# Kernel tuning notes

Measured on AMD Instinct MI355X. Metric: run time of the kernel, lower is better.

The kernel has to match this reference:

```python
import math
import jax, jax.numpy as jnp
import numpy as np

N, E = 20000, 640000
S_DIM, Z_DIM, H, QK, VD = 64, 64, 4, 8, 8
EPS = 1e-8


def quat_rotate(v, q):
    # v: [..., 3], q: [..., 4] (w, x, y, z), broadcastable. Unit-quaternion rotation:
    # v' = v + 2*(w*(u x v) + u x (u x v))
    w = q[..., 0:1]
    u = q[..., 1:4]
    uv = jnp.cross(u, v)
    return v + 2.0 * (w * uv + jnp.cross(u, uv))


def setup_inputs() -> dict:
    key = jax.random.key(0)
    ks = jax.random.split(key, 16)
    s = jax.random.normal(ks[0], (N, S_DIM), dtype=jnp.float32)
    z = jax.random.normal(ks[1], (E, Z_DIM), dtype=jnp.float32)
    edge_index = jax.random.randint(ks[2], (2, E), 0, N)
    quaternion = jax.random.normal(ks[3], (N, 4), dtype=jnp.float32)
    quaternion = quaternion / jnp.linalg.norm(quaternion, axis=-1, keepdims=True)
    translation = jax.random.normal(ks[4], (N, 3), dtype=jnp.float32)
    sc_s = 1.0 / math.sqrt(S_DIM)
    sc_z = 1.0 / math.sqrt(Z_DIM)
    # weights stored [in, out] so y = x @ W (equivalent to torch x @ W.T)
    Wq_s = jax.random.normal(ks[5], (S_DIM, H * S_DIM), dtype=jnp.float32) * sc_s
    Wk_s = jax.random.normal(ks[6], (S_DIM, H * S_DIM), dtype=jnp.float32) * sc_s
    Wv_s = jax.random.normal(ks[7], (S_DIM, H * S_DIM), dtype=jnp.float32) * sc_s
    Wq_v = jax.random.normal(ks[8], (S_DIM, H * QK * 3), dtype=jnp.float32) * sc_s
    Wk_v = jax.random.normal(ks[9], (S_DIM, H * QK * 3), dtype=jnp.float32) * sc_s
    Wv_v = jax.random.normal(ks[10], (S_DIM, H * VD * 3), dtype=jnp.float32) * sc_s
    Wb = jax.random.normal(ks[11], (Z_DIM, H), dtype=jnp.float32) * sc_z
    bb = jnp.zeros((H,), dtype=jnp.float32)
    Wdz = jax.random.normal(ks[12], (Z_DIM, Z_DIM // 4), dtype=jnp.float32) * sc_z
    bdz = jnp.zeros((Z_DIM // 4,), dtype=jnp.float32)
    head_weights = jnp.full((H,), 0.541324854612918, dtype=jnp.float32)  # softplus^{-1}(1)
    concat_dim = Z_DIM // 4 + S_DIM + VD * 4
    Wout = jax.random.normal(ks[13], (H * concat_dim, S_DIM), dtype=jnp.float32) / math.sqrt(H * concat_dim)
    bout = jnp.zeros((S_DIM,), dtype=jnp.float32)
    return {
        's': s, 'z': z, 'edge_index': edge_index, 'quaternion': quaternion,
        'translation': translation, 'Wq_s': Wq_s, 'Wk_s': Wk_s, 'Wv_s': Wv_s,
        'Wq_v': Wq_v, 'Wk_v': Wk_v, 'Wv_v': Wv_v, 'Wb': Wb, 'bb': bb,
        'Wdz': Wdz, 'bdz': bdz, 'head_weights': head_weights,
        'Wout': Wout, 'bout': bout,
    }


def reference(s, z, edge_index, quaternion, translation,
              Wq_s, Wk_s, Wv_s, Wq_v, Wk_v, Wv_v,
              Wb, bb, Wdz, bdz, head_weights, Wout, bout):
    idx_i, idx_j = edge_index[0], edge_index[1]
    n = s.shape[0]
    h = head_weights.shape[0]
    qk = Wq_v.shape[1] // (3 * h)
    vd = Wv_v.shape[1] // (3 * h)

    q_scalar = (s @ Wq_s).reshape(n, h, -1)
    k_scalar = (s @ Wk_s).reshape(n, h, -1)
    v_scalar = (s @ Wv_s).reshape(n, h, -1)

    def to_points(x):
        # torch.split into 3 chunks then stack(dim=-1): [n, 3*c] -> [n, c, 3]
        c = x.shape[-1] // 3
        return jnp.swapaxes(x.reshape(n, 3, c), 1, 2)

    quat_b = quaternion[:, None, :]
    trans_b = translation[:, None, :]
    q_vec = (quat_rotate(to_points(s @ Wq_v), quat_b) + trans_b).reshape(n, h, qk, 3)
    k_vec = (quat_rotate(to_points(s @ Wk_v), quat_b) + trans_b).reshape(n, h, qk, 3)
    v_vec = (quat_rotate(to_points(s @ Wv_v), quat_b) + trans_b).reshape(n, h, vd, 3)

    b_bias = z @ Wb + bb  # [E, H]

    attn = jnp.sum(k_scalar[idx_i] * q_scalar[idx_j], axis=-1)  # [E, H]
    attn = attn * math.sqrt(1.0 / 3 * qk) + math.sqrt(1.0 / 3) * b_bias

    disp = q_vec[idx_i] - k_vec[idx_j]            # [E, H, qk, 3]
    vec_att = jnp.sum(disp * disp, axis=-1)       # [E, H, qk]
    hw = jax.nn.softplus(head_weights)[None, :, None]
    vec_att = jnp.sum(vec_att * hw, axis=-1) * math.sqrt(1.0 / (3 * (qk * 9.0 / 2))) * (-0.5)
    attn = attn + vec_att

    # segment softmax over destination node idx_i
    seg_max = jax.ops.segment_max(attn, idx_i, num_segments=n)
    ea = jnp.exp(attn - seg_max[idx_i])
    denom = jax.ops.segment_sum(ea, idx_i, num_segments=n)
    attn = ea / denom[idx_i]                      # [E, H]

    out_scalar = jax.ops.segment_sum(attn[:, :, None] * v_scalar[idx_i], idx_i, num_segments=n)
    out_scalar = out_scalar.reshape(n, -1)

    out_vec = jax.ops.segment_sum(attn[:, :, None, None] * v_vec[idx_i], idx_i, num_segments=n)
    out_vec = out_vec - translation[:, None, None, :]
    q_conj = jnp.concatenate([quaternion[:, :1], -quaternion[:, 1:]], axis=-1)
    out_vec = quat_rotate(out_vec, q_conj[:, None, None, :])   # [n, h, vd, 3]
    out_vec_norm = jnp.sqrt(jnp.sum(out_vec * out_vec, axis=-1) + EPS).reshape(n, -1)
    out_vec_flat = out_vec.reshape(n, -1, 3)

    pair_z = z @ Wdz + bdz                         # [E, z/4]
    out_pair = jax.ops.segment_sum(attn[:, :, None] * pair_z[:, None, :], idx_i, num_segments=n)
    out_pair = out_pair.reshape(n, -1)

    feats = jnp.concatenate([out_scalar,
                             out_vec_flat[..., 0], out_vec_flat[..., 1], out_vec_flat[..., 2],
                             out_vec_norm, out_pair], axis=-1)
    return feats @ Wout + bout
```

## Files before the change

### kernel.cpp

```cpp
#include <hip/hip_runtime.h>
#include <stdint.h>


#define C_SQRT83  1.6329931618554518f
#define C_SQRT13  0.5773502691896258f
#define C_VEC    -0.04811252243246881f

__device__ __forceinline__ unsigned short f2bf(float f){
  unsigned u = __float_as_uint(f);
  u += 0x7fffu + ((u >> 16) & 1u);
  return (unsigned short)(u >> 16);
}
__device__ __forceinline__ unsigned pack2(float a, float b){
  return (unsigned)f2bf(a) | ((unsigned)f2bf(b) << 16);
}
__device__ __forceinline__ float bflo(unsigned u){ return __uint_as_float(u << 16); }
__device__ __forceinline__ float bfhi(unsigned u){ return __uint_as_float(u & 0xffff0000u); }

__device__ __forceinline__ void quat_rot(float w, float ux, float uy, float uz,
                                         float vx, float vy, float vz,
                                         float& ox, float& oy, float& oz){
  float cx = uy*vz - uz*vy;
  float cy = uz*vx - ux*vz;
  float cz = ux*vy - uy*vx;
  float dx = uy*cz - uz*cy;
  float dy = uz*cx - ux*cz;
  float dz = ux*cy - uy*cx;
  ox = vx + 2.f*(w*cx + dx);
  oy = vy + 2.f*(w*cy + dy);
  oz = vz + 2.f*(w*cz + dz);
}


__global__ __launch_bounds__(256) void k_zero(unsigned* __restrict__ counts, int n){
  int g = blockIdx.x*256 + threadIdx.x;
  if (g < n) counts[g] = 0u;
}

__global__ __launch_bounds__(256) void k_count(const int* __restrict__ ei,
                                               unsigned* __restrict__ counts, int ne){
  int e = blockIdx.x*256 + threadIdx.x;
  if (e >= ne) return;
  atomicAdd(&counts[ei[e]], 1u);
}

__global__ __launch_bounds__(256) void k_scan(const unsigned* __restrict__ counts,
                                              unsigned* __restrict__ row_off,
                                              unsigned* __restrict__ cursor, int n){
  __shared__ unsigned part[256];
  int t = threadIdx.x;
  int chunk = (n + 255) >> 8;
  int s0 = t*chunk, s1 = min(s0 + chunk, n);
  unsigned sum = 0;
  for (int k = s0; k < s1; ++k) sum += counts[k];
  part[t] = sum; __syncthreads();
  for (int off = 1; off < 256; off <<= 1){
    unsigned v = (t >= off) ? part[t-off] : 0u;
    __syncthreads();
    part[t] += v;
    __syncthreads();
  }
  unsigned run = (t == 0) ? 0u : part[t-1];
  for (int k = s0; k < s1; ++k){
    row_off[k] = run; cursor[k] = run; run += counts[k];
  }
  if (t == 255) row_off[n] = part[255];
}

__global__ __launch_bounds__(256) void k_fill(const int* __restrict__ ei,
                                              unsigned* __restrict__ cursor,
                                              unsigned* __restrict__ si,
                                              unsigned* __restrict__ sj,
                                              unsigned* __restrict__ se, int ne){
  int e = blockIdx.x*256 + threadIdx.x;
  if (e >= ne) return;
  int i = ei[e];
  unsigned pos = atomicAdd(&cursor[i], 1u);
  si[pos] = (unsigned)i;
  sj[pos] = (unsigned)ei[ne + e];
  se[pos] = (unsigned)e;
}


#define BN 32

__device__ __forceinline__ void pass256(const float* __restrict__ W,
                                        const float st[BN][66], int cg, int sl,
                                        float acc[8][4]){
  #pragma unroll
  for (int i=0;i<8;i++){ acc[i][0]=0.f; acc[i][1]=0.f; acc[i][2]=0.f; acc[i][3]=0.f; }
  #pragma unroll 4
  for (int k = 0; k < 64; ++k){
    const float4 w = *(const float4*)(W + (size_t)k*256 + cg*4);
    #pragma unroll
    for (int i=0;i<8;i++){
      const float sv = st[sl*8+i][k];
      acc[i][0] += sv*w.x; acc[i][1] += sv*w.y; acc[i][2] += sv*w.z; acc[i][3] += sv*w.w;
    }
  }
}

__device__ __forceinline__ void pass96(const float* __restrict__ W,
                                       const float st[BN][66], int cgp, int slp,
                                       float acc[4][4]){
  #pragma unroll
  for (int i=0;i<4;i++){ acc[i][0]=0.f; acc[i][1]=0.f; acc[i][2]=0.f; acc[i][3]=0.f; }
  if (cgp >= 24) return;
  #pragma unroll 4
  for (int k = 0; k < 64; ++k){
    const float4 w = *(const float4*)(W + (size_t)k*96 + cgp*4);
    #pragma unroll
    for (int i=0;i<4;i++){
      const float sv = st[slp*4+i][k];
      acc[i][0] += sv*w.x; acc[i][1] += sv*w.y; acc[i][2] += sv*w.z; acc[i][3] += sv*w.w;
    }
  }
}

__global__ __launch_bounds__(256) void k_proj(
    const float* __restrict__ s, const float* __restrict__ quat, const float* __restrict__ trans,
    const float* __restrict__ Wqs, const float* __restrict__ Wks, const float* __restrict__ Wvs,
    const float* __restrict__ Wqv, const float* __restrict__ Wkv, const float* __restrict__ Wvv,
    unsigned* __restrict__ qs, unsigned* __restrict__ ks, float* __restrict__ vs,
    unsigned* __restrict__ qv, unsigned* __restrict__ kv, float* __restrict__ vv, int n)
{
  __shared__ float st[BN][66];
  __shared__ float pt[BN][97];
  const int tid = threadIdx.x;
  const int node0 = blockIdx.x * BN;

  #pragma unroll
  for (int r = 0; r < 2; ++r){
    const int idx = tid + r*256;
    const int nd = idx >> 4, c4 = idx & 15;
    const int g = node0 + nd;
    float4 v = make_float4(0.f,0.f,0.f,0.f);
    if (g < n) v = *(const float4*)(s + (size_t)g*64 + c4*4);
    st[nd][c4*4+0]=v.x; st[nd][c4*4+1]=v.y; st[nd][c4*4+2]=v.z; st[nd][c4*4+3]=v.w;
  }
  __syncthreads();

  const int cg = tid & 63, sl = tid >> 6;
  const int cgp = tid & 31, slp = tid >> 5;
  float acc[8][4];

  pass256(Wqs, st, cg, sl, acc);
  #pragma unroll
  for (int i=0;i<8;i++){
    const int g = node0 + sl*8 + i;
    if (g < n){
      uint2 u; u.x = pack2(acc[i][0],acc[i][1]); u.y = pack2(acc[i][2],acc[i][3]);
      *(uint2*)(qs + (size_t)g*128 + cg*2) = u;
    }
  }
  pass256(Wks, st, cg, sl, acc);
  #pragma unroll
  for (int i=0;i<8;i++){
    const int g = node0 + sl*8 + i;
    if (g < n){
      uint2 u; u.x = pack2(acc[i][0],acc[i][1]); u.y = pack2(acc[i][2],acc[i][3]);
      *(uint2*)(ks + (size_t)g*128 + cg*2) = u;
    }
  }
  pass256(Wvs, st, cg, sl, acc);
  #pragma unroll
  for (int i=0;i<8;i++){
    const int g = node0 + sl*8 + i;
    if (g < n){
      float4 f; f.x=acc[i][0]; f.y=acc[i][1]; f.z=acc[i][2]; f.w=acc[i][3];
      *(float4*)(vs + (size_t)g*256 + cg*4) = f;
    }
  }

  float pac[4][4];

  pass96(Wqv, st, cgp, slp, pac);
  __syncthreads();
  if (cgp < 24){
    #pragma unroll
    for (int i=0;i<4;i++){
      #pragma unroll
      for (int c=0;c<4;c++) pt[slp*4+i][cgp*4+c] = pac[i][c];
    }
  }
  __syncthreads();
  #pragma unroll
  for (int r = 0; r < 2; ++r){
    const int t2 = tid + r*256;
    const int nd = t2 >> 4, pp = t2 & 15;
    const int g = node0 + nd;
    if (g < n){
      const float4 q4 = *(const float4*)(quat + (size_t)g*4);
      const float tx = trans[(size_t)g*3], ty = trans[(size_t)g*3+1], tz = trans[(size_t)g*3+2];
      float x0,y0,z0,x1,y1,z1;
      quat_rot(q4.x,q4.y,q4.z,q4.w, pt[nd][2*pp],   pt[nd][32+2*pp],   pt[nd][64+2*pp],   x0,y0,z0);
      quat_rot(q4.x,q4.y,q4.z,q4.w, pt[nd][2*pp+1], pt[nd][32+2*pp+1], pt[nd][64+2*pp+1], x1,y1,z1);
      x0+=tx; y0+=ty; z0+=tz; x1+=tx; y1+=ty; z1+=tz;
      unsigned* d = qv + (size_t)g*48 + pp*3;
      d[0] = pack2(x0,y0); d[1] = pack2(z0,x1); d[2] = pack2(y1,z1);
    }
  }

  pass96(Wkv, st, cgp, slp, pac);
  __syncthreads();
  if (cgp < 24){
    #pragma unroll
    for (int i=0;i<4;i++){
      #pragma unroll
      for (int c=0;c<4;c++) pt[slp*4+i][cgp*4+c] = pac[i][c];
    }
  }
  __syncthreads();
  #pragma unroll
  for (int r = 0; r < 2; ++r){
    const int t2 = tid + r*256;
    const int nd = t2 >> 4, pp = t2 & 15;
    const int g = node0 + nd;
    if (g < n){
      const float4 q4 = *(const float4*)(quat + (size_t)g*4);
      const float tx = trans[(size_t)g*3], ty = trans[(size_t)g*3+1], tz = trans[(size_t)g*3+2];
      float x0,y0,z0,x1,y1,z1;
      quat_rot(q4.x,q4.y,q4.z,q4.w, pt[nd][2*pp],   pt[nd][32+2*pp],   pt[nd][64+2*pp],   x0,y0,z0);
      quat_rot(q4.x,q4.y,q4.z,q4.w, pt[nd][2*pp+1], pt[nd][32+2*pp+1], pt[nd][64+2*pp+1], x1,y1,z1);
      x0+=tx; y0+=ty; z0+=tz; x1+=tx; y1+=ty; z1+=tz;
      unsigned* d = kv + (size_t)g*48 + pp*3;
      d[0] = pack2(x0,y0); d[1] = pack2(z0,x1); d[2] = pack2(y1,z1);
    }
  }

  pass96(Wvv, st, cgp, slp, pac);
  __syncthreads();
  if (cgp < 24){
    #pragma unroll
    for (int i=0;i<4;i++){
      #pragma unroll
      for (int c=0;c<4;c++) pt[slp*4+i][cgp*4+c] = pac[i][c];
    }
  }
  __syncthreads();
  #pragma unroll
  for (int r = 0; r < 12; ++r){
    const int idx = tid + r*256;
    const int nd = idx / 96, col = idx - nd*96;
    const int g = node0 + nd;
    if (g < n) vv[(size_t)g*96 + col] = pt[nd][col];
  }
}


__global__ __launch_bounds__(256) void k_edge(
    const float* __restrict__ z,
    const unsigned* __restrict__ si, const unsigned* __restrict__ sj, const unsigned* __restrict__ se,
    const float* __restrict__ Wb,  const float* __restrict__ bb,
    const float* __restrict__ Wdz, const float* __restrict__ bdz,
    const float* __restrict__ hwts,
    const unsigned* __restrict__ qs, const unsigned* __restrict__ ks,
    const unsigned* __restrict__ qv, const unsigned* __restrict__ kv,
    float* __restrict__ logits, unsigned* __restrict__ pz, int ne)
{
  const int p = blockIdx.x*256 + threadIdx.x;
  if (p >= ne) return;
  const unsigned i = si[p], j = sj[p], e = se[p];

  float b4[4];  b4[0]=b4[1]=b4[2]=b4[3]=0.f;
  float pacc[16];
  #pragma unroll
  for (int c=0;c<16;c++) pacc[c]=0.f;
  const float* zr = z + (size_t)e*64;
  #pragma unroll
  for (int k4 = 0; k4 < 16; ++k4){
    const float4 zv = *(const float4*)(zr + 4*k4);
    #pragma unroll
    for (int kk = 0; kk < 4; ++kk){
      const int k = 4*k4 + kk;
      const float zk = (kk==0)?zv.x:((kk==1)?zv.y:((kk==2)?zv.z:zv.w));
      const float4 wb = *(const float4*)(Wb + k*4);
      b4[0]+=zk*wb.x; b4[1]+=zk*wb.y; b4[2]+=zk*wb.z; b4[3]+=zk*wb.w;
      const float* wd = Wdz + k*16;
      const float4 w0=*(const float4*)(wd), w1=*(const float4*)(wd+4),
                   w2=*(const float4*)(wd+8), w3=*(const float4*)(wd+12);
      pacc[ 0]+=zk*w0.x; pacc[ 1]+=zk*w0.y; pacc[ 2]+=zk*w0.z; pacc[ 3]+=zk*w0.w;
      pacc[ 4]+=zk*w1.x; pacc[ 5]+=zk*w1.y; pacc[ 6]+=zk*w1.z; pacc[ 7]+=zk*w1.w;
      pacc[ 8]+=zk*w2.x; pacc[ 9]+=zk*w2.y; pacc[10]+=zk*w2.z; pacc[11]+=zk*w2.w;
      pacc[12]+=zk*w3.x; pacc[13]+=zk*w3.y; pacc[14]+=zk*w3.z; pacc[15]+=zk*w3.w;
    }
  }
  #pragma unroll
  for (int c=0;c<16;c++) pacc[c] += bdz[c];
  { uint4 u0, u1;
    u0.x=pack2(pacc[0],pacc[1]);   u0.y=pack2(pacc[2],pacc[3]);
    u0.z=pack2(pacc[4],pacc[5]);   u0.w=pack2(pacc[6],pacc[7]);
    u1.x=pack2(pacc[8],pacc[9]);   u1.y=pack2(pacc[10],pacc[11]);
    u1.z=pack2(pacc[12],pacc[13]); u1.w=pack2(pacc[14],pacc[15]);
    uint4* d = (uint4*)(pz + (size_t)p*8);
    d[0]=u0; d[1]=u1; }

  const uint4* kr = (const uint4*)(ks + (size_t)i*128);
  const uint4* qr = (const uint4*)(qs + (size_t)j*128);
  float sdot[4];
  #pragma unroll
  for (int h = 0; h < 4; ++h){
    float acc = 0.f;
    #pragma unroll
    for (int c = 0; c < 8; ++c){
      const uint4 a = kr[h*8+c];
      const uint4 b = qr[h*8+c];
      acc += bflo(a.x)*bflo(b.x) + bfhi(a.x)*bfhi(b.x);
      acc += bflo(a.y)*bflo(b.y) + bfhi(a.y)*bfhi(b.y);
      acc += bflo(a.z)*bflo(b.z) + bfhi(a.z)*bfhi(b.z);
      acc += bflo(a.w)*bflo(b.w) + bfhi(a.w)*bfhi(b.w);
    }
    sdot[h] = acc;
  }

  const uint4* qvr = (const uint4*)(qv + (size_t)i*48);
  const uint4* kvr = (const uint4*)(kv + (size_t)j*48);
  float vsum[4];
  #pragma unroll
  for (int h = 0; h < 4; ++h){
    float acc = 0.f;
    #pragma unroll
    for (int c = 0; c < 3; ++c){
      const uint4 a = qvr[h*3+c];
      const uint4 b = kvr[h*3+c];
      float d;
      d = bflo(a.x)-bflo(b.x); acc += d*d;  d = bfhi(a.x)-bfhi(b.x); acc += d*d;
      d = bflo(a.y)-bflo(b.y); acc += d*d;  d = bfhi(a.y)-bfhi(b.y); acc += d*d;
      d = bflo(a.z)-bflo(b.z); acc += d*d;  d = bfhi(a.z)-bfhi(b.z); acc += d*d;
      d = bflo(a.w)-bflo(b.w); acc += d*d;  d = bfhi(a.w)-bfhi(b.w); acc += d*d;
    }
    vsum[h] = acc;
  }

  float4 lg;
  {
    float l[4];
    #pragma unroll
    for (int h = 0; h < 4; ++h){
      const float hw = log1pf(__expf(hwts[h]));
      l[h] = C_SQRT83*sdot[h] + C_SQRT13*(b4[h] + bb[h]) + C_VEC*hw*vsum[h];
    }
    lg.x=l[0]; lg.y=l[1]; lg.z=l[2]; lg.w=l[3];
  }
  *(float4*)(logits + (size_t)p*4) = lg;
}


__global__ __launch_bounds__(256) void k_soft(
    const float* __restrict__ logits, const unsigned* __restrict__ pz,
    const unsigned* __restrict__ row_off, float* __restrict__ out_pair, int n)
{
  const int t = blockIdx.x*256 + threadIdx.x;
  if (t >= n*4) return;
  const int i = t >> 2, h = t & 3;
  const int beg = (int)row_off[i], end = (int)row_off[i+1];

  float m = -3.4e38f;
  for (int p = beg; p < end; ++p) m = fmaxf(m, logits[(size_t)p*4 + h]);

  float ssum = 0.f;
  float acc[16];
  #pragma unroll
  for (int c=0;c<16;c++) acc[c]=0.f;

  for (int p = beg; p < end; ++p){
    const float w = __expf(logits[(size_t)p*4 + h] - m);
    ssum += w;
    const uint4* pr = (const uint4*)(pz + (size_t)p*8);
    const uint4 a = pr[0], b = pr[1];
    acc[ 0]+=w*bflo(a.x); acc[ 1]+=w*bfhi(a.x);
    acc[ 2]+=w*bflo(a.y); acc[ 3]+=w*bfhi(a.y);
    acc[ 4]+=w*bflo(a.z); acc[ 5]+=w*bfhi(a.z);
    acc[ 6]+=w*bflo(a.w); acc[ 7]+=w*bfhi(a.w);
    acc[ 8]+=w*bflo(b.x); acc[ 9]+=w*bfhi(b.x);
    acc[10]+=w*bflo(b.y); acc[11]+=w*bfhi(b.y);
    acc[12]+=w*bflo(b.z); acc[13]+=w*bfhi(b.z);
    acc[14]+=w*bflo(b.w); acc[15]+=w*bfhi(b.w);
  }
  const float inv = (end > beg) ? (1.f/ssum) : 0.f;
  float4* dst = (float4*)(out_pair + (size_t)i*64 + h*16);
  float4 o;
  o.x=acc[0]*inv;  o.y=acc[1]*inv;  o.z=acc[2]*inv;  o.w=acc[3]*inv;  dst[0]=o;
  o.x=acc[4]*inv;  o.y=acc[5]*inv;  o.z=acc[6]*inv;  o.w=acc[7]*inv;  dst[1]=o;
  o.x=acc[8]*inv;  o.y=acc[9]*inv;  o.z=acc[10]*inv; o.w=acc[11]*inv; dst[2]=o;
  o.x=acc[12]*inv; o.y=acc[13]*inv; o.z=acc[14]*inv; o.w=acc[15]*inv; dst[3]=o;
}


__global__ __launch_bounds__(256) void k_out(
    const float* __restrict__ vs, const float* __restrict__ vv,
    const float* __restrict__ out_pair, const unsigned* __restrict__ row_off,
    const float* __restrict__ quat, const float* __restrict__ trans,
    const float* __restrict__ Wout, const float* __restrict__ bout,
    float* __restrict__ out, int n)
{
  __shared__ float feats[32][448];
  __shared__ int degs[32];
  const int tid = threadIdx.x;
  const int node0 = blockIdx.x*32;

  if (tid < 32){
    const int g = node0 + tid;
    degs[tid] = (g < n) ? (int)(row_off[g+1] - row_off[g]) : 1;
  }
  __syncthreads();

  for (int x = tid; x < 32*256; x += 256){
    const int nd = x >> 8, c = x & 255;
    const int g = node0 + nd;
    feats[nd][c] = (g < n && degs[nd] > 0) ? vs[(size_t)g*256 + c] : 0.f;
  }
  for (int x = tid; x < 32*64; x += 256){
    const int nd = x >> 6, c = x & 63;
    const int g = node0 + nd;
    feats[nd][384 + c] = (g < n) ? out_pair[(size_t)g*64 + c] : 0.f;
  }
  for (int x = tid; x < 32*32; x += 256){
    const int nd = x >> 5, pt = x & 31;
    const int g = node0 + nd;
    float X=0.f, Y=0.f, Z=0.f;
    if (g < n){
      if (degs[nd] > 0){
        X = vv[(size_t)g*96 + pt];
        Y = vv[(size_t)g*96 + 32 + pt];
        Z = vv[(size_t)g*96 + 64 + pt];
      } else {
        const float4 q4 = *(const float4*)(quat + (size_t)g*4);
        const float tx = trans[(size_t)g*3], ty = trans[(size_t)g*3+1], tz = trans[(size_t)g*3+2];
        quat_rot(q4.x, -q4.y, -q4.z, -q4.w, -tx, -ty, -tz, X, Y, Z);
      }
    }
    feats[nd][256 + pt] = X;
    feats[nd][288 + pt] = Y;
    feats[nd][320 + pt] = Z;
    feats[nd][352 + pt] = sqrtf(X*X + Y*Y + Z*Z + 1e-8f);
  }
  __syncthreads();

  const int lane = tid & 63;
  const int wave = tid >> 6;
  float acc[8];
  #pragma unroll
  for (int q8=0;q8<8;q8++) acc[q8]=0.f;

  for (int k = 0; k < 448; ++k){
    const float wv = Wout[(size_t)k*64 + lane];
    #pragma unroll
    for (int q8 = 0; q8 < 8; ++q8)
      acc[q8] += feats[wave*8 + q8][k] * wv;
  }
  const float bo = bout[lane];
  #pragma unroll
  for (int q8 = 0; q8 < 8; ++q8){
    const int g = node0 + wave*8 + q8;
    if (g < n) out[(size_t)g*64 + lane] = acc[q8] + bo;
  }
}


extern "C" void kernel_launch(void* const* d_in, const int* in_sizes, int n_in,
                              void* d_out, int out_size, void* d_ws, size_t ws_size,
                              hipStream_t stream) {
  const float* s     = (const float*)d_in[0];
  const float* z     = (const float*)d_in[1];
  const int*   ei    = (const int*)  d_in[2];
  const float* quat  = (const float*)d_in[3];
  const float* trans = (const float*)d_in[4];
  const float* Wqs   = (const float*)d_in[5];
  const float* Wks   = (const float*)d_in[6];
  const float* Wvs   = (const float*)d_in[7];
  const float* Wqv   = (const float*)d_in[8];
  const float* Wkv   = (const float*)d_in[9];
  const float* Wvv   = (const float*)d_in[10];
  const float* Wb    = (const float*)d_in[11];
  const float* bb    = (const float*)d_in[12];
  const float* Wdz   = (const float*)d_in[13];
  const float* bdz   = (const float*)d_in[14];
  const float* hwts  = (const float*)d_in[15];
  const float* Wout  = (const float*)d_in[16];
  const float* bout  = (const float*)d_in[17];
  float* out = (float*)d_out;

  const int n  = in_sizes[0] / 64;
  const int ne = in_sizes[1] / 64;

  size_t off = 0;
  char* base = (char*)d_ws;
  auto take = [&](size_t bytes)->char* {
    char* p = base + off;
    off += (bytes + 255) & ~(size_t)255;
    return p;
  };
  unsigned* qs     = (unsigned*)take((size_t)n*512);
  unsigned* ks     = (unsigned*)take((size_t)n*512);
  unsigned* qvt    = (unsigned*)take((size_t)n*192);
  unsigned* kvt    = (unsigned*)take((size_t)n*192);
  float*    vs     = (float*)   take((size_t)n*1024);
  float*    vv     = (float*)   take((size_t)n*384);
  float*    logits = (float*)   take((size_t)ne*16);
  unsigned* pz     = (unsigned*)take((size_t)ne*32);
  unsigned* counts = (unsigned*)take((size_t)n*4);
  unsigned* roff   = (unsigned*)take((size_t)(n+1)*4);
  unsigned* cur    = (unsigned*)take((size_t)n*4);
  unsigned* si     = (unsigned*)take((size_t)ne*4);
  unsigned* sj     = (unsigned*)take((size_t)ne*4);
  unsigned* se     = (unsigned*)take((size_t)ne*4);
  float*    opair  = (float*)   take((size_t)n*256);
  (void)ws_size; (void)n_in; (void)out_size;

  const int gbE = (ne + 255) / 256;
  const int gbN = (n  + 255) / 256;

  k_zero <<<gbN, 256, 0, stream>>>(counts, n);
  k_count<<<gbE, 256, 0, stream>>>(ei, counts, ne);
  k_scan <<<1,   256, 0, stream>>>(counts, roff, cur, n);
  k_fill <<<gbE, 256, 0, stream>>>(ei, cur, si, sj, se, ne);
  k_proj <<<(n + BN - 1)/BN, 256, 0, stream>>>(s, quat, trans, Wqs, Wks, Wvs, Wqv, Wkv, Wvv,
                                               qs, ks, vs, qvt, kvt, vv, n);
  k_edge <<<gbE, 256, 0, stream>>>(z, si, sj, se, Wb, bb, Wdz, bdz, hwts,
                                   qs, ks, qvt, kvt, logits, pz, ne);
  k_soft <<<(n*4 + 255)/256, 256, 0, stream>>>(logits, pz, roff, opair, n);
  k_out  <<<(n + 31)/32, 256, 0, stream>>>(vs, vv, opair, roff, quat, trans,
                                           Wout, bout, out, n);
}
```

Baseline: 688.1 us.

## Use wave-per-node softmax, atomic-free CSR fill, transposed smem projection, vectorized output GEMV

The CSR build now records each edge's rank from the counting atomic, so the fill step computes positions without a second atomic pass. The zero kernel is replaced by hipMemsetAsync. The projection kernel stores node features transposed in shared memory so it can use float4 LDS reads. The segment softmax now gives each node a full wave with shuffle reductions instead of one thread per (node, head), which spreads work more evenly but computes exp more than once per edge. The output GEMV reads four feature values at a time as float4.

```diff
diff --git a/kernel.cpp b/kernel.cpp
--- a/kernel.cpp
+++ b/kernel.cpp
@@ -32,21 +32,16 @@
 }
 
 
-__global__ __launch_bounds__(256) void k_zero(unsigned* __restrict__ counts, int n){
-  int g = blockIdx.x*256 + threadIdx.x;
-  if (g < n) counts[g] = 0u;
-}
-
 __global__ __launch_bounds__(256) void k_count(const int* __restrict__ ei,
-                                               unsigned* __restrict__ counts, int ne){
+                                               unsigned* __restrict__ counts,
+                                               unsigned* __restrict__ rank, int ne){
   int e = blockIdx.x*256 + threadIdx.x;
   if (e >= ne) return;
-  atomicAdd(&counts[ei[e]], 1u);
+  rank[e] = atomicAdd(&counts[ei[e]], 1u);
 }
 
 __global__ __launch_bounds__(256) void k_scan(const unsigned* __restrict__ counts,
-                                              unsigned* __restrict__ row_off,
-                                              unsigned* __restrict__ cursor, int n){
+                                              unsigned* __restrict__ row_off, int n){
   __shared__ unsigned part[256];
   int t = threadIdx.x;
   int chunk = (n + 255) >> 8;
@@ -62,20 +57,21 @@
   }
   unsigned run = (t == 0) ? 0u : part[t-1];
   for (int k = s0; k < s1; ++k){
-    row_off[k] = run; cursor[k] = run; run += counts[k];
+    row_off[k] = run; run += counts[k];
   }
   if (t == 255) row_off[n] = part[255];
 }
 
 __global__ __launch_bounds__(256) void k_fill(const int* __restrict__ ei,
-                                              unsigned* __restrict__ cursor,
+                                              const unsigned* __restrict__ rank,
+                                              const unsigned* __restrict__ roff,
                                               unsigned* __restrict__ si,
                                               unsigned* __restrict__ sj,
                                               unsigned* __restrict__ se, int ne){
   int e = blockIdx.x*256 + threadIdx.x;
   if (e >= ne) return;
-  int i = ei[e];
-  unsigned pos = atomicAdd(&cursor[i], 1u);
+  const int i = ei[e];
+  const unsigned pos = roff[i] + rank[e];
   si[pos] = (unsigned)i;
   sj[pos] = (unsigned)ei[ne + e];
   se[pos] = (unsigned)e;
@@ -85,23 +81,28 @@
 #define BN 32
 
 __device__ __forceinline__ void pass256(const float* __restrict__ W,
-                                        const float st[BN][66], int cg, int sl,
+                                        const float stT[64][40], int cg, int sl,
                                         float acc[8][4]){
   #pragma unroll
   for (int i=0;i<8;i++){ acc[i][0]=0.f; acc[i][1]=0.f; acc[i][2]=0.f; acc[i][3]=0.f; }
   #pragma unroll 4
   for (int k = 0; k < 64; ++k){
-    const float4 w = *(const float4*)(W + (size_t)k*256 + cg*4);
-    #pragma unroll
-    for (int i=0;i<8;i++){
-      const float sv = st[sl*8+i][k];
-      acc[i][0] += sv*w.x; acc[i][1] += sv*w.y; acc[i][2] += sv*w.z; acc[i][3] += sv*w.w;
-    }
+    const float4 w  = *(const float4*)(W + (size_t)k*256 + cg*4);
+    const float4 n0 = *(const float4*)&stT[k][sl*8];
+    const float4 n1 = *(const float4*)&stT[k][sl*8+4];
+    acc[0][0]+=n0.x*w.x; acc[0][1]+=n0.x*w.y; acc[0][2]+=n0.x*w.z; acc[0][3]+=n0.x*w.w;
+    acc[1][0]+=n0.y*w.x; acc[1][1]+=n0.y*w.y; acc[1][2]+=n0.y*w.z; acc[1][3]+=n0.y*w.w;
+    acc[2][0]+=n0.z*w.x; acc[2][1]+=n0.z*w.y; acc[2][2]+=n0.z*w.z; acc[2][3]+=n0.z*w.w;
+    acc[3][0]+=n0.w*w.x; acc[3][1]+=n0.w*w.y; acc[3][2]+=n0.w*w.z; acc[3][3]+=n0.w*w.w;
+    acc[4][0]+=n1.x*w.x; acc[4][1]+=n1.x*w.y; acc[4][2]+=n1.x*w.z; acc[4][3]+=n1.x*w.w;
+    acc[5][0]+=n1.y*w.x; acc[5][1]+=n1.y*w.y; acc[5][2]+=n1.y*w.z; acc[5][3]+=n1.y*w.w;
+    acc[6][0]+=n1.z*w.x; acc[6][1]+=n1.z*w.y; acc[6][2]+=n1.z*w.z; acc[6][3]+=n1.z*w.w;
+    acc[7][0]+=n1.w*w.x; acc[7][1]+=n1.w*w.y; acc[7][2]+=n1.w*w.z; acc[7][3]+=n1.w*w.w;
   }
 }
 
 __device__ __forceinline__ void pass96(const float* __restrict__ W,
-                                       const float st[BN][66], int cgp, int slp,
+                                       const float stT[64][40], int cgp, int slp,
                                        float acc[4][4]){
   #pragma unroll
   for (int i=0;i<4;i++){ acc[i][0]=0.f; acc[i][1]=0.f; acc[i][2]=0.f; acc[i][3]=0.f; }
@@ -109,11 +110,11 @@
   #pragma unroll 4
   for (int k = 0; k < 64; ++k){
     const float4 w = *(const float4*)(W + (size_t)k*96 + cgp*4);
-    #pragma unroll
-    for (int i=0;i<4;i++){
-      const float sv = st[slp*4+i][k];
-      acc[i][0] += sv*w.x; acc[i][1] += sv*w.y; acc[i][2] += sv*w.z; acc[i][3] += sv*w.w;
-    }
+    const float4 nv = *(const float4*)&stT[k][slp*4];
+    acc[0][0]+=nv.x*w.x; acc[0][1]+=nv.x*w.y; acc[0][2]+=nv.x*w.z; acc[0][3]+=nv.x*w.w;
+    acc[1][0]+=nv.y*w.x; acc[1][1]+=nv.y*w.y; acc[1][2]+=nv.y*w.z; acc[1][3]+=nv.y*w.w;
+    acc[2][0]+=nv.z*w.x; acc[2][1]+=nv.z*w.y; acc[2][2]+=nv.z*w.z; acc[2][3]+=nv.z*w.w;
+    acc[3][0]+=nv.w*w.x; acc[3][1]+=nv.w*w.y; acc[3][2]+=nv.w*w.z; acc[3][3]+=nv.w*w.w;
   }
 }
 
@@ -124,7 +125,7 @@
     unsigned* __restrict__ qs, unsigned* __restrict__ ks, float* __restrict__ vs,
     unsigned* __restrict__ qv, unsigned* __restrict__ kv, float* __restrict__ vv, int n)
 {
-  __shared__ float st[BN][66];
+  __shared__ float stT[64][40];
   __shared__ float pt[BN][97];
   const int tid = threadIdx.x;
   const int node0 = blockIdx.x * BN;
@@ -136,7 +137,7 @@
     const int g = node0 + nd;
     float4 v = make_float4(0.f,0.f,0.f,0.f);
     if (g < n) v = *(const float4*)(s + (size_t)g*64 + c4*4);
-    st[nd][c4*4+0]=v.x; st[nd][c4*4+1]=v.y; st[nd][c4*4+2]=v.z; st[nd][c4*4+3]=v.w;
+    stT[c4*4+0][nd]=v.x; stT[c4*4+1][nd]=v.y; stT[c4*4+2][nd]=v.z; stT[c4*4+3][nd]=v.w;
   }
   __syncthreads();
 
@@ -144,7 +145,7 @@
   const int cgp = tid & 31, slp = tid >> 5;
   float acc[8][4];
 
-  pass256(Wqs, st, cg, sl, acc);
+  pass256(Wqs, stT, cg, sl, acc);
   #pragma unroll
   for (int i=0;i<8;i++){
     const int g = node0 + sl*8 + i;
@@ -153,7 +154,7 @@
       *(uint2*)(qs + (size_t)g*128 + cg*2) = u;
     }
   }
-  pass256(Wks, st, cg, sl, acc);
+  pass256(Wks, stT, cg, sl, acc);
   #pragma unroll
   for (int i=0;i<8;i++){
     const int g = node0 + sl*8 + i;
@@ -162,7 +163,7 @@
       *(uint2*)(ks + (size_t)g*128 + cg*2) = u;
     }
   }
-  pass256(Wvs, st, cg, sl, acc);
+  pass256(Wvs, stT, cg, sl, acc);
   #pragma unroll
   for (int i=0;i<8;i++){
     const int g = node0 + sl*8 + i;
@@ -174,7 +175,7 @@
 
   float pac[4][4];
 
-  pass96(Wqv, st, cgp, slp, pac);
+  pass96(Wqv, stT, cgp, slp, pac);
   __syncthreads();
   if (cgp < 24){
     #pragma unroll
@@ -201,7 +202,7 @@
     }
   }
 
-  pass96(Wkv, st, cgp, slp, pac);
+  pass96(Wkv, stT, cgp, slp, pac);
   __syncthreads();
   if (cgp < 24){
     #pragma unroll
@@ -228,7 +229,7 @@
     }
   }
 
-  pass96(Wvv, st, cgp, slp, pac);
+  pass96(Wvv, stT, cgp, slp, pac);
   __syncthreads();
   if (cgp < 24){
     #pragma unroll
@@ -350,40 +351,57 @@
     const float* __restrict__ logits, const unsigned* __restrict__ pz,
     const unsigned* __restrict__ row_off, float* __restrict__ out_pair, int n)
 {
-  const int t = blockIdx.x*256 + threadIdx.x;
-  if (t >= n*4) return;
-  const int i = t >> 2, h = t & 3;
-  const int beg = (int)row_off[i], end = (int)row_off[i+1];
-
-  float m = -3.4e38f;
-  for (int p = beg; p < end; ++p) m = fmaxf(m, logits[(size_t)p*4 + h]);
-
-  float ssum = 0.f;
-  float acc[16];
-  #pragma unroll
-  for (int c=0;c<16;c++) acc[c]=0.f;
-
-  for (int p = beg; p < end; ++p){
-    const float w = __expf(logits[(size_t)p*4 + h] - m);
-    ssum += w;
-    const uint4* pr = (const uint4*)(pz + (size_t)p*8);
-    const uint4 a = pr[0], b = pr[1];
-    acc[ 0]+=w*bflo(a.x); acc[ 1]+=w*bfhi(a.x);
-    acc[ 2]+=w*bflo(a.y); acc[ 3]+=w*bfhi(a.y);
-    acc[ 4]+=w*bflo(a.z); acc[ 5]+=w*bfhi(a.z);
-    acc[ 6]+=w*bflo(a.w); acc[ 7]+=w*bfhi(a.w);
-    acc[ 8]+=w*bflo(b.x); acc[ 9]+=w*bfhi(b.x);
-    acc[10]+=w*bflo(b.y); acc[11]+=w*bfhi(b.y);
-    acc[12]+=w*bflo(b.z); acc[13]+=w*bfhi(b.z);
-    acc[14]+=w*bflo(b.w); acc[15]+=w*bfhi(b.w);
-  }
-  const float inv = (end > beg) ? (1.f/ssum) : 0.f;
-  float4* dst = (float4*)(out_pair + (size_t)i*64 + h*16);
-  float4 o;
-  o.x=acc[0]*inv;  o.y=acc[1]*inv;  o.z=acc[2]*inv;  o.w=acc[3]*inv;  dst[0]=o;
-  o.x=acc[4]*inv;  o.y=acc[5]*inv;  o.z=acc[6]*inv;  o.w=acc[7]*inv;  dst[1]=o;
-  o.x=acc[8]*inv;  o.y=acc[9]*inv;  o.z=acc[10]*inv; o.w=acc[11]*inv; dst[2]=o;
-  o.x=acc[12]*inv; o.y=acc[13]*inv; o.z=acc[14]*inv; o.w=acc[15]*inv; dst[3]=o;
+  const int node = blockIdx.x*4 + (threadIdx.x >> 6);
+  if (node >= n) return;
+  const int lane = threadIdx.x & 63;
+  const int beg = (int)row_off[node], end = (int)row_off[node+1];
+
+  float m[4] = {-3.0e38f,-3.0e38f,-3.0e38f,-3.0e38f};
+  for (int p = beg + lane; p < end; p += 64){
+    const float4 l = *(const float4*)(logits + (size_t)p*4);
+    m[0]=fmaxf(m[0],l.x); m[1]=fmaxf(m[1],l.y); m[2]=fmaxf(m[2],l.z); m[3]=fmaxf(m[3],l.w);
+  }
+  #pragma unroll
+  for (int msk = 1; msk < 64; msk <<= 1){
+    #pragma unroll
+    for (int h=0;h<4;h++) m[h] = fmaxf(m[h], __shfl_xor(m[h], msk));
+  }
+  float S[4] = {0.f,0.f,0.f,0.f};
+  for (int p = beg + lane; p < end; p += 64){
+    const float4 l = *(const float4*)(logits + (size_t)p*4);
+    S[0]+=__expf(l.x-m[0]); S[1]+=__expf(l.y-m[1]);
+    S[2]+=__expf(l.z-m[2]); S[3]+=__expf(l.w-m[3]);
+  }
+  #pragma unroll
+  for (int msk = 1; msk < 64; msk <<= 1){
+    #pragma unroll
+    for (int h=0;h<4;h++) S[h] += __shfl_xor(S[h], msk);
+  }
+  float inv[4];
+  #pragma unroll
+  for (int h=0;h<4;h++) inv[h] = (S[h] > 0.f) ? (1.f/S[h]) : 0.f;
+
+  const int e4 = lane >> 4, c = lane & 15;
+  float acc[4] = {0.f,0.f,0.f,0.f};
+  for (int base = beg; base < end; base += 4){
+    const int p = base + e4;
+    if (p < end){
+      const float4 l = *(const float4*)(logits + (size_t)p*4);
+      const unsigned u = pz[(size_t)p*8 + (c>>1)];
+      const float pzv = (c & 1) ? bfhi(u) : bflo(u);
+      acc[0] += __expf(l.x-m[0]) * pzv;
+      acc[1] += __expf(l.y-m[1]) * pzv;
+      acc[2] += __expf(l.z-m[2]) * pzv;
+      acc[3] += __expf(l.w-m[3]) * pzv;
+    }
+  }
+  #pragma unroll
+  for (int msk = 16; msk < 64; msk <<= 1){
+    #pragma unroll
+    for (int h=0;h<4;h++) acc[h] += __shfl_xor(acc[h], msk);
+  }
+  const int hOut = lane >> 4;
+  out_pair[(size_t)node*64 + lane] = acc[hOut] * inv[hOut];
 }
 
 
@@ -443,11 +461,16 @@
   #pragma unroll
   for (int q8=0;q8<8;q8++) acc[q8]=0.f;
 
-  for (int k = 0; k < 448; ++k){
-    const float wv = Wout[(size_t)k*64 + lane];
-    #pragma unroll
-    for (int q8 = 0; q8 < 8; ++q8)
-      acc[q8] += feats[wave*8 + q8][k] * wv;
+  for (int k0 = 0; k0 < 448; k0 += 4){
+    const float w0 = Wout[(size_t)(k0+0)*64 + lane];
+    const float w1 = Wout[(size_t)(k0+1)*64 + lane];
+    const float w2 = Wout[(size_t)(k0+2)*64 + lane];
+    const float w3 = Wout[(size_t)(k0+3)*64 + lane];
+    #pragma unroll
+    for (int q8 = 0; q8 < 8; ++q8){
+      const float4 f = *(const float4*)&feats[wave*8 + q8][k0];
+      acc[q8] += f.x*w0 + f.y*w1 + f.z*w2 + f.w*w3;
+    }
   }
   const float bo = bout[lane];
   #pragma unroll
@@ -501,7 +524,7 @@
   unsigned* pz     = (unsigned*)take((size_t)ne*32);
   unsigned* counts = (unsigned*)take((size_t)n*4);
   unsigned* roff   = (unsigned*)take((size_t)(n+1)*4);
-  unsigned* cur    = (unsigned*)take((size_t)n*4);
+  unsigned* rank   = (unsigned*)take((size_t)ne*4);
   unsigned* si     = (unsigned*)take((size_t)ne*4);
   unsigned* sj     = (unsigned*)take((size_t)ne*4);
   unsigned* se     = (unsigned*)take((size_t)ne*4);
@@ -509,17 +532,16 @@
   (void)ws_size; (void)n_in; (void)out_size;
 
   const int gbE = (ne + 255) / 256;
-  const int gbN = (n  + 255) / 256;
-
-  k_zero <<<gbN, 256, 0, stream>>>(counts, n);
-  k_count<<<gbE, 256, 0, stream>>>(ei, counts, ne);
-  k_scan <<<1,   256, 0, stream>>>(counts, roff, cur, n);
-  k_fill <<<gbE, 256, 0, stream>>>(ei, cur, si, sj, se, ne);
+
+  hipMemsetAsync(counts, 0, (size_t)n*4, stream);
+  k_count<<<gbE, 256, 0, stream>>>(ei, counts, rank, ne);
+  k_scan <<<1,   256, 0, stream>>>(counts, roff, n);
+  k_fill <<<gbE, 256, 0, stream>>>(ei, rank, roff, si, sj, se, ne);
   k_proj <<<(n + BN - 1)/BN, 256, 0, stream>>>(s, quat, trans, Wqs, Wks, Wvs, Wqv, Wkv, Wvv,
                                                qs, ks, vs, qvt, kvt, vv, n);
   k_edge <<<gbE, 256, 0, stream>>>(z, si, sj, se, Wb, bb, Wdz, bdz, hwts,
                                    qs, ks, qvt, kvt, logits, pz, ne);
-  k_soft <<<(n*4 + 255)/256, 256, 0, stream>>>(logits, pz, roff, opair, n);
+  k_soft <<<(n + 3)/4, 256, 0, stream>>>(logits, pz, roff, opair, n);
   k_out  <<<(n + 31)/32, 256, 0, stream>>>(vs, vv, opair, roff, quat, trans,
                                            Wout, bout, out, n);
 }
```

Measured after the change: 659.8 us. -4.1%, faster.
